# Kernel optimization log

Hardware: AMD Instinct MI355X
Metric: run time of the kernel (lower is better)

Reference implementation:

```python
import jax, jax.numpy as jnp
import numpy as np

EPS = 1e-10
NUM_RELATION = 4
N_NODES = 50000
N_EDGES = 800000
D_IN = 128
D_H = 256


def rgc_layer(x, src, dst, rel, rel_w, rel_b, loop_w, loop_b):
    # torchdrug RelationalGraphConv: scatter-mean per (node, relation), then
    # linear over concatenated per-relation features + self-loop linear + relu.
    N, d = x.shape
    msg = x[src]                                      # [E, d] gather
    idx = dst * NUM_RELATION + rel                    # [E] bucket per (node, relation)
    num_seg = N * NUM_RELATION
    agg = jax.ops.segment_sum(msg, idx, num_segments=num_seg)            # [N*R, d]
    cnt = jax.ops.segment_sum(jnp.ones((msg.shape[0], 1), x.dtype), idx,
                              num_segments=num_seg)                       # [N*R, 1]
    update = (agg / (cnt + EPS)).reshape(N, NUM_RELATION * d)            # [N, R*d]
    out = update @ rel_w + rel_b + x @ loop_w + loop_b                   # [N, d_out]
    return jax.nn.relu(out)


def highway(x, hp_w, hp_b, ht_w, ht_b):
    proj = jax.nn.relu(x @ hp_w + hp_b)
    gate = jax.nn.sigmoid(x @ ht_w + ht_b)
    return gate * proj + (1.0 - gate) * x


def setup_inputs() -> dict:
    key = jax.random.key(0)
    ks = jax.random.split(key, 16)
    s = 0.02
    inp = {
        "x": jax.random.normal(ks[0], (N_NODES, D_IN), dtype=jnp.float32),
        "src": jax.random.randint(ks[1], (N_EDGES,), 0, N_NODES, dtype=jnp.int32),
        "dst": jax.random.randint(ks[2], (N_EDGES,), 0, N_NODES, dtype=jnp.int32),
        "rel": jax.random.randint(ks[3], (N_EDGES,), 0, NUM_RELATION, dtype=jnp.int32),
        # layer 1: RGC(128->256) + Highway(256)
        "rel_w1": jax.random.normal(ks[4], (NUM_RELATION * D_IN, D_H), dtype=jnp.float32) * s,
        "rel_b1": jnp.zeros((D_H,), jnp.float32),
        "loop_w1": jax.random.normal(ks[5], (D_IN, D_H), dtype=jnp.float32) * s,
        "loop_b1": jnp.zeros((D_H,), jnp.float32),
        "hp_w1": jax.random.normal(ks[6], (D_H, D_H), dtype=jnp.float32) * s,
        "hp_b1": jnp.zeros((D_H,), jnp.float32),
        "ht_w1": jax.random.normal(ks[7], (D_H, D_H), dtype=jnp.float32) * s,
        "ht_b1": jnp.full((D_H,), -2.0, jnp.float32),  # transform.bias.data.fill_(-2.0)
        # layer 2: RGC(256->256) + Highway(256)
        "rel_w2": jax.random.normal(ks[8], (NUM_RELATION * D_H, D_H), dtype=jnp.float32) * s,
        "rel_b2": jnp.zeros((D_H,), jnp.float32),
        "loop_w2": jax.random.normal(ks[9], (D_H, D_H), dtype=jnp.float32) * s,
        "loop_b2": jnp.zeros((D_H,), jnp.float32),
        "hp_w2": jax.random.normal(ks[10], (D_H, D_H), dtype=jnp.float32) * s,
        "hp_b2": jnp.zeros((D_H,), jnp.float32),
        "ht_w2": jax.random.normal(ks[11], (D_H, D_H), dtype=jnp.float32) * s,
        "ht_b2": jnp.full((D_H,), -2.0, jnp.float32),
    }
    return inp


def reference(x, src, dst, rel,
              rel_w1, rel_b1, loop_w1, loop_b1, hp_w1, hp_b1, ht_w1, ht_b1,
              rel_w2, rel_b2, loop_w2, loop_b2, hp_w2, hp_b2, ht_w2, ht_b2):
    h = rgc_layer(x, src, dst, rel, rel_w1, rel_b1, loop_w1, loop_b1)
    h = highway(h, hp_w1, hp_b1, ht_w1, ht_b1)
    h = rgc_layer(h, src, dst, rel, rel_w2, rel_b2, loop_w2, loop_b2)
    h = highway(h, hp_w2, hp_b2, ht_w2, ht_b2)
    return h  # node_feature, shape [N, 256]
```

## Files before the change

kernel.cpp:

```cpp
#include <hip/hip_runtime.h>

typedef __bf16 bf16_t;
typedef __bf16 bf16x8 __attribute__((ext_vector_type(8)));
typedef __bf16 bf16x4 __attribute__((ext_vector_type(4)));
typedef float f32x4 __attribute__((ext_vector_type(4)));
typedef int i32x4 __attribute__((ext_vector_type(4)));

#define BM 128
#define BK 64

__device__ __forceinline__ void gload_lds16(const void* g, void* s) {
    __builtin_amdgcn_global_load_lds(
        (const __attribute__((address_space(1))) unsigned int*)g,
        (__attribute__((address_space(3))) unsigned int*)s, 16, 0, 0);
}

__global__ __launch_bounds__(256, 2) void gemm_k(
    const bf16_t* __restrict__ A, int lda, int M,
    const bf16_t* __restrict__ Bt, int K,
    const float* __restrict__ bias, int relu_flag,
    bf16_t* __restrict__ outb, int ldo, int ocol,
    int NTM)
{
    __shared__ __align__(16) bf16_t As[BM * BK];
    __shared__ __align__(16) bf16_t Bs[256 * BK];

    const int L   = blockIdx.x;
    const int xcd = L & 7;
    const int sup = L >> 3;
    const int mt  = sup * 8 + xcd;
    if (mt >= NTM) return;
    const int m0 = mt * BM;

    const int tid  = threadIdx.x;
    const int wave = tid >> 6, lane = tid & 63;
    const int wr   = wave >> 1, wc = wave & 1;
    const int lm   = lane & 15, quad = lane >> 4;

    const bf16_t* ag[4];
    const bf16_t* bg[8];
    #pragma unroll
    for (int j = 0; j < 4; j++) {
        int c   = j * 256 + tid;
        int row = c >> 3;
        int col = ((c & 7) ^ (row & 7)) << 3;
        int gm  = m0 + row; if (gm >= M) gm = M - 1;
        ag[j] = A + (size_t)gm * lda + col;
    }
    #pragma unroll
    for (int j = 0; j < 8; j++) {
        int c   = j * 256 + tid;
        int row = c >> 3;
        int col = ((c & 7) ^ (row & 7)) << 3;
        bg[j] = Bt + (size_t)row * K + col;
    }

    f32x4 acc[4][8] = {};

    for (int k0 = 0; k0 < K; k0 += BK) {
        __syncthreads();
        #pragma unroll
        for (int j = 0; j < 4; j++)
            gload_lds16(ag[j] + k0, As + (size_t)(j * 256 + tid) * 8);
        #pragma unroll
        for (int j = 0; j < 8; j++)
            gload_lds16(bg[j] + k0, Bs + (size_t)(j * 256 + tid) * 8);
        __syncthreads();

        #pragma unroll
        for (int h = 0; h < 2; h++) {
            bf16x8 af[4];
            #pragma unroll
            for (int i = 0; i < 4; i++) {
                int r = wr * 64 + i * 16 + lm;
                af[i] = *(const bf16x8*)&As[(size_t)(r * 8 + ((h * 4 + quad) ^ (r & 7))) * 8];
            }
            #pragma unroll
            for (int ni = 0; ni < 8; ni++) {
                int r = wc * 128 + ni * 16 + lm;
                bf16x8 bfr = *(const bf16x8*)&Bs[(size_t)(r * 8 + ((h * 4 + quad) ^ (r & 7))) * 8];
                #pragma unroll
                for (int mi = 0; mi < 4; mi++)
                    acc[mi][ni] = __builtin_amdgcn_mfma_f32_16x16x32_bf16(
                        af[mi], bfr, acc[mi][ni], 0, 0, 0);
            }
        }
    }

    #pragma unroll
    for (int mi = 0; mi < 4; mi++) {
        #pragma unroll
        for (int ni = 0; ni < 8; ni++) {
            int col = wc * 128 + ni * 16 + lm;
            float b = bias[col];
            #pragma unroll
            for (int r = 0; r < 4; r++) {
                int row = m0 + wr * 64 + mi * 16 + quad * 4 + r;
                if (row < M) {
                    float v = acc[mi][ni][r] + b;
                    if (relu_flag) v = fmaxf(v, 0.f);
                    outb[(size_t)row * ldo + ocol + col] = (bf16_t)v;
                }
            }
        }
    }
}

__global__ __launch_bounds__(256, 2) void gemm_hw2(
    const bf16_t* __restrict__ A, int M,
    const bf16_t* __restrict__ Bt,
    const float* __restrict__ bias,
    bf16_t* __restrict__ outb, int ldo, int ocol,
    float* __restrict__ outf, int NTM)
{
    __shared__ __align__(16) bf16_t As[128 * 64];
    __shared__ __align__(16) bf16_t Bs[256 * 64];

    const int L    = blockIdx.x;
    const int xcd  = L & 7;
    const int rest = L >> 3;
    const int nt   = rest & 1;
    const int sup  = rest >> 1;
    const int mt   = sup * 8 + xcd;
    if (mt >= NTM) return;
    const int m0 = mt * 128;

    const int tid  = threadIdx.x;
    const int wave = tid >> 6, lane = tid & 63;
    const int lm   = lane & 15, quad = lane >> 4;

    const bf16_t* ag[4];
    const bf16_t* bg[8];
    #pragma unroll
    for (int j = 0; j < 4; j++) {
        int c   = j * 256 + tid;
        int row = c >> 3;
        int col = ((c & 7) ^ (row & 7)) << 3;
        int gm  = m0 + row; if (gm >= M) gm = M - 1;
        ag[j] = A + (size_t)gm * 256 + col;
    }
    #pragma unroll
    for (int j = 0; j < 8; j++) {
        int c    = j * 256 + tid;
        int row  = c >> 3;
        int col  = ((c & 7) ^ (row & 7)) << 3;
        int grow = nt * 128 + row + ((row >= 128) ? 128 : 0);
        bg[j] = Bt + (size_t)grow * 256 + col;
    }

    f32x4 acc[2][16] = {};

    for (int k0 = 0; k0 < 256; k0 += 64) {
        __syncthreads();
        #pragma unroll
        for (int j = 0; j < 4; j++)
            gload_lds16(ag[j] + k0, As + (size_t)(j * 256 + tid) * 8);
        #pragma unroll
        for (int j = 0; j < 8; j++)
            gload_lds16(bg[j] + k0, Bs + (size_t)(j * 256 + tid) * 8);
        __syncthreads();

        #pragma unroll
        for (int h = 0; h < 2; h++) {
            bf16x8 af[2];
            #pragma unroll
            for (int i = 0; i < 2; i++) {
                int r = wave * 32 + i * 16 + lm;
                af[i] = *(const bf16x8*)&As[(size_t)(r * 8 + ((h * 4 + quad) ^ (r & 7))) * 8];
            }
            #pragma unroll
            for (int ni = 0; ni < 16; ni++) {
                int r = ni * 16 + lm;
                bf16x8 bfr = *(const bf16x8*)&Bs[(size_t)(r * 8 + ((h * 4 + quad) ^ (r & 7))) * 8];
                #pragma unroll
                for (int mi = 0; mi < 2; mi++)
                    acc[mi][ni] = __builtin_amdgcn_mfma_f32_16x16x32_bf16(
                        af[mi], bfr, acc[mi][ni], 0, 0, 0);
            }
        }
    }

    #pragma unroll
    for (int mi = 0; mi < 2; mi++) {
        #pragma unroll
        for (int ni = 0; ni < 8; ni++) {
            int col = nt * 128 + ni * 16 + lm;
            float bp  = bias[col];
            float bg2 = bias[256 + col];
            #pragma unroll
            for (int r = 0; r < 4; r++) {
                int row = m0 + wave * 32 + mi * 16 + quad * 4 + r;
                if (row < M) {
                    float p = acc[mi][ni][r] + bp;
                    float g = acc[mi][ni + 8][r] + bg2;
                    float s = 1.0f / (1.0f + __expf(-g));
                    float hv = (float)A[(size_t)row * 256 + col];
                    float v = s * fmaxf(p, 0.f) + (1.0f - s) * hv;
                    if (outf) outf[(size_t)row * 256 + col] = v;
                    else      outb[(size_t)row * ldo + ocol + col] = (bf16_t)v;
                }
            }
        }
    }
}

__global__ void prep_all(
    const float* __restrict__ rel_w1, const float* __restrict__ loop_w1,
    const float* __restrict__ rel_w2, const float* __restrict__ loop_w2,
    const float* __restrict__ hp_w1,  const float* __restrict__ ht_w1,
    const float* __restrict__ hp_w2,  const float* __restrict__ ht_w2,
    bf16_t* __restrict__ W1t, bf16_t* __restrict__ W2t,
    bf16_t* __restrict__ Wh1t, bf16_t* __restrict__ Wh2t,
    const float* __restrict__ rb1, const float* __restrict__ lb1,
    const float* __restrict__ rb2, const float* __restrict__ lb2,
    const float* __restrict__ hpb1, const float* __restrict__ htb1,
    const float* __restrict__ hpb2, const float* __restrict__ htb2,
    float* __restrict__ bR1, float* __restrict__ bR2,
    float* __restrict__ bH1, float* __restrict__ bH2,
    const float* __restrict__ x, bf16_t* __restrict__ A1, int N,
    int* __restrict__ cnt, int NSEG, int cvb)
{
    int b = blockIdx.x, tid = threadIdx.x;
    if (b < 2944) {
        const float* W; bf16_t* Wt; int ldk, k0, n0, base;
        if      (b < 512)  { W = rel_w1;  Wt = W1t;  ldk = 640;  k0 = 0;    n0 = 0;   base = 0; }
        else if (b < 640)  { W = loop_w1; Wt = W1t;  ldk = 640;  k0 = 512;  n0 = 0;   base = 512; }
        else if (b < 1664) { W = rel_w2;  Wt = W2t;  ldk = 1280; k0 = 0;    n0 = 0;   base = 640; }
        else if (b < 1920) { W = loop_w2; Wt = W2t;  ldk = 1280; k0 = 1024; n0 = 0;   base = 1664; }
        else if (b < 2176) { W = hp_w1;   Wt = Wh1t; ldk = 256;  k0 = 0;    n0 = 0;   base = 1920; }
        else if (b < 2432) { W = ht_w1;   Wt = Wh1t; ldk = 256;  k0 = 0;    n0 = 256; base = 2176; }
        else if (b < 2688) { W = hp_w2;   Wt = Wh2t; ldk = 256;  k0 = 0;    n0 = 0;   base = 2432; }
        else               { W = ht_w2;   Wt = Wh2t; ldk = 256;  k0 = 0;    n0 = 256; base = 2688; }
        int k = b - base;
        int n = tid;
        Wt[(size_t)(n0 + n) * ldk + k0 + k] = (bf16_t)W[(size_t)k * 256 + n];
    } else if (b == 2944) {
        int t = tid;
        bR1[t] = rb1[t] + lb1[t];
        bR2[t] = rb2[t] + lb2[t];
        bH1[t] = hpb1[t]; bH1[256 + t] = htb1[t];
        bH2[t] = hpb2[t]; bH2[256 + t] = htb2[t];
    } else if (b < 2945 + cvb) {
        int t = (b - 2945) * 256 + tid;
        if (t < N * 32) {
            int row = t >> 5, c = (t & 31) << 2;
            f32x4 v = *(const f32x4*)(x + (size_t)row * 128 + c);
            bf16x4 o;
            o[0] = (bf16_t)v[0]; o[1] = (bf16_t)v[1]; o[2] = (bf16_t)v[2]; o[3] = (bf16_t)v[3];
            *(bf16x4*)(A1 + (size_t)row * 640 + 512 + c) = o;
        }
    } else {
        int t = ((b - 2945 - cvb) * 256 + tid) * 4;
        if (t < NSEG) {
            i32x4 z = {0, 0, 0, 0};
            *(i32x4*)(cnt + t) = z;
        }
    }
}

__global__ void count_k(const int* __restrict__ dst, const int* __restrict__ rel,
                        int* __restrict__ cnt, int E)
{
    int e = blockIdx.x * blockDim.x + threadIdx.x;
    if (e < E) atomicAdd(&cnt[dst[e] * 4 + rel[e]], 1);
}

__global__ void scan_partial(const int* __restrict__ cnt, int* __restrict__ offs,
                             int* __restrict__ chunkSums, int NSEG)
{
    __shared__ int sh[256];
    int t = threadIdx.x;
    int idx = blockIdx.x * 256 + t;
    int v = (idx < NSEG) ? cnt[idx] : 0;
    sh[t] = v;
    __syncthreads();
    for (int d = 1; d < 256; d <<= 1) {
        int add = (t >= d) ? sh[t - d] : 0;
        __syncthreads();
        sh[t] += add;
        __syncthreads();
    }
    if (idx < NSEG) offs[idx] = sh[t] - v;
    if (t == 255) chunkSums[blockIdx.x] = sh[t];
}

__global__ void scan_chunks(int* __restrict__ chunkSums, int NCHUNK)
{
    __shared__ int sh[1024];
    int t = threadIdx.x;
    int v = (t < NCHUNK) ? chunkSums[t] : 0;
    sh[t] = v;
    __syncthreads();
    for (int d = 1; d < 1024; d <<= 1) {
        int add = (t >= d) ? sh[t - d] : 0;
        __syncthreads();
        sh[t] += add;
        __syncthreads();
    }
    if (t < NCHUNK) chunkSums[t] = sh[t] - v;
}

__global__ void scan_add(int* __restrict__ offs, const int* __restrict__ chunkSums,
                         int* __restrict__ cursor, int NSEG)
{
    int idx = blockIdx.x * 256 + threadIdx.x;
    if (idx < NSEG) {
        int o = offs[idx] + chunkSums[blockIdx.x];
        offs[idx] = o;
        cursor[idx] = o;
    }
}

__global__ void fill_k(const int* __restrict__ src, const int* __restrict__ dst,
                       const int* __restrict__ rel,
                       int* __restrict__ cursor, int* __restrict__ eidx, int E)
{
    int e = blockIdx.x * blockDim.x + threadIdx.x;
    if (e < E) {
        int seg = dst[e] * 4 + rel[e];
        int pos = atomicAdd(&cursor[seg], 1);
        eidx[pos] = src[e];
    }
}

__global__ void seg_mean256(const int* __restrict__ offs, const int* __restrict__ cnt,
                            const int* __restrict__ eidx,
                            const bf16_t* __restrict__ xb, int ldx,
                            bf16_t* __restrict__ Aout, int lda, int NSEG)
{
    int wv = (blockIdx.x << 2) + (threadIdx.x >> 6);
    if (wv >= NSEG) return;
    int lane = threadIdx.x & 63;
    int half = lane >> 5;
    int c = (lane & 31) << 3;
    int start = offs[wv];
    int n = cnt[wv];
    float acc[8] = {};
    int i = 0;
    for (; i + 8 <= n; i += 8) {
        int s0 = eidx[start + i + 0 + half];
        int s1 = eidx[start + i + 2 + half];
        int s2 = eidx[start + i + 4 + half];
        int s3 = eidx[start + i + 6 + half];
        bf16x8 v0 = *(const bf16x8*)(xb + (size_t)s0 * ldx + c);
        bf16x8 v1 = *(const bf16x8*)(xb + (size_t)s1 * ldx + c);
        bf16x8 v2 = *(const bf16x8*)(xb + (size_t)s2 * ldx + c);
        bf16x8 v3 = *(const bf16x8*)(xb + (size_t)s3 * ldx + c);
        #pragma unroll
        for (int j = 0; j < 8; j++)
            acc[j] += ((float)v0[j] + (float)v1[j]) + ((float)v2[j] + (float)v3[j]);
    }
    for (; i + 2 <= n; i += 2) {
        int s = eidx[start + i + half];
        bf16x8 v = *(const bf16x8*)(xb + (size_t)s * ldx + c);
        #pragma unroll
        for (int j = 0; j < 8; j++) acc[j] += (float)v[j];
    }
    if (i < n && half == 0) {
        int s = eidx[start + i];
        bf16x8 v = *(const bf16x8*)(xb + (size_t)s * ldx + c);
        #pragma unroll
        for (int j = 0; j < 8; j++) acc[j] += (float)v[j];
    }
    #pragma unroll
    for (int j = 0; j < 8; j++) acc[j] += __shfl_xor(acc[j], 32, 64);
    if (half == 0) {
        float inv = 1.0f / ((float)n + 1e-10f);
        int node = wv >> 2, r = wv & 3;
        bf16x8 o;
        #pragma unroll
        for (int j = 0; j < 8; j++) o[j] = (bf16_t)(acc[j] * inv);
        *(bf16x8*)(Aout + (size_t)node * lda + r * 256 + c) = o;
    }
}

__global__ void seg_mean128(const int* __restrict__ offs, const int* __restrict__ cnt,
                            const int* __restrict__ eidx,
                            const bf16_t* __restrict__ xb, int ldx,
                            bf16_t* __restrict__ Aout, int lda, int NSEG)
{
    int wv = (blockIdx.x << 2) + (threadIdx.x >> 6);
    if (wv >= NSEG) return;
    int lane = threadIdx.x & 63;
    int q = lane >> 4;
    int c = (lane & 15) << 3;
    int start = offs[wv];
    int n = cnt[wv];
    float acc[8] = {};
    int i = 0;
    for (; i + 8 <= n; i += 8) {
        int s0 = eidx[start + i + q];
        int s1 = eidx[start + i + 4 + q];
        bf16x8 v0 = *(const bf16x8*)(xb + (size_t)s0 * ldx + c);
        bf16x8 v1 = *(const bf16x8*)(xb + (size_t)s1 * ldx + c);
        #pragma unroll
        for (int j = 0; j < 8; j++) acc[j] += (float)v0[j] + (float)v1[j];
    }
    for (; i + 4 <= n; i += 4) {
        int s = eidx[start + i + q];
        bf16x8 v = *(const bf16x8*)(xb + (size_t)s * ldx + c);
        #pragma unroll
        for (int j = 0; j < 8; j++) acc[j] += (float)v[j];
    }
    if (q < n - i) {
        int s = eidx[start + i + q];
        bf16x8 v = *(const bf16x8*)(xb + (size_t)s * ldx + c);
        #pragma unroll
        for (int j = 0; j < 8; j++) acc[j] += (float)v[j];
    }
    #pragma unroll
    for (int j = 0; j < 8; j++) {
        acc[j] += __shfl_xor(acc[j], 16, 64);
        acc[j] += __shfl_xor(acc[j], 32, 64);
    }
    if (lane < 16) {
        float inv = 1.0f / ((float)n + 1e-10f);
        int node = wv >> 2, r = wv & 3;
        bf16x8 o;
        #pragma unroll
        for (int j = 0; j < 8; j++) o[j] = (bf16_t)(acc[j] * inv);
        *(bf16x8*)(Aout + (size_t)node * lda + r * 128 + c) = o;
    }
}

extern "C" void kernel_launch(void* const* d_in, const int* in_sizes, int n_in,
                              void* d_out, int out_size, void* d_ws, size_t ws_size,
                              hipStream_t stream)
{
    const float* x       = (const float*)d_in[0];
    const int*   src     = (const int*)d_in[1];
    const int*   dst     = (const int*)d_in[2];
    const int*   rel     = (const int*)d_in[3];
    const float* rel_w1  = (const float*)d_in[4];
    const float* rel_b1  = (const float*)d_in[5];
    const float* loop_w1 = (const float*)d_in[6];
    const float* loop_b1 = (const float*)d_in[7];
    const float* hp_w1   = (const float*)d_in[8];
    const float* hp_b1   = (const float*)d_in[9];
    const float* ht_w1   = (const float*)d_in[10];
    const float* ht_b1   = (const float*)d_in[11];
    const float* rel_w2  = (const float*)d_in[12];
    const float* rel_b2  = (const float*)d_in[13];
    const float* loop_w2 = (const float*)d_in[14];
    const float* loop_b2 = (const float*)d_in[15];
    const float* hp_w2   = (const float*)d_in[16];
    const float* hp_b2   = (const float*)d_in[17];
    const float* ht_w2   = (const float*)d_in[18];
    const float* ht_b2   = (const float*)d_in[19];

    const int N = in_sizes[0] / 128;
    const int E = in_sizes[1];
    const int NSEG = N * 4;
    const int NCHUNK = (NSEG + 255) / 256;
    float* out = (float*)d_out;

    char* ws = (char*)d_ws;
    size_t off = 0;
    auto alloc = [&](size_t bytes) {
        void* p = ws + off;
        off += (bytes + 255) & ~(size_t)255;
        return p;
    };
    int*    cnt    = (int*)alloc((size_t)NSEG * 4);
    int*    offs   = (int*)alloc((size_t)NSEG * 4);
    int*    cursor = (int*)alloc((size_t)NSEG * 4);
    int*    chunkS = (int*)alloc(4096);
    int*    eidx   = (int*)alloc((size_t)E * 4);
    bf16_t* A1     = (bf16_t*)alloc((size_t)N * 640 * 2);
    bf16_t* A2     = (bf16_t*)alloc((size_t)N * 1280 * 2);
    bf16_t* h      = (bf16_t*)alloc((size_t)N * 256 * 2);
    bf16_t* W1t    = (bf16_t*)alloc((size_t)256 * 640 * 2);
    bf16_t* W2t    = (bf16_t*)alloc((size_t)256 * 1280 * 2);
    bf16_t* Wh1t   = (bf16_t*)alloc((size_t)512 * 256 * 2);
    bf16_t* Wh2t   = (bf16_t*)alloc((size_t)512 * 256 * 2);
    float*  bR1    = (float*)alloc(256 * 4);
    float*  bR2    = (float*)alloc(256 * 4);
    float*  bH1    = (float*)alloc(512 * 4);
    float*  bH2    = (float*)alloc(512 * 4);

    dim3 blk(256);
    const int NTM = (N + BM - 1) / BM;
    const int supers = (NTM + 7) / 8;
    const int gridRGC = supers * 8;
    const int gridHW  = supers * 8 * 2;

    const int cvb = (N * 32 + 255) / 256;
    const int zb  = (NSEG / 4 + 255) / 256;
    prep_all<<<dim3(2945 + cvb + zb), blk, 0, stream>>>(
        rel_w1, loop_w1, rel_w2, loop_w2, hp_w1, ht_w1, hp_w2, ht_w2,
        W1t, W2t, Wh1t, Wh2t,
        rel_b1, loop_b1, rel_b2, loop_b2, hp_b1, ht_b1, hp_b2, ht_b2,
        bR1, bR2, bH1, bH2,
        x, A1, N, cnt, NSEG, cvb);

    count_k<<<dim3((E + 255) / 256), blk, 0, stream>>>(dst, rel, cnt, E);
    scan_partial<<<dim3(NCHUNK), blk, 0, stream>>>(cnt, offs, chunkS, NSEG);
    scan_chunks<<<dim3(1), dim3(1024), 0, stream>>>(chunkS, NCHUNK);
    scan_add<<<dim3(NCHUNK), blk, 0, stream>>>(offs, chunkS, cursor, NSEG);
    fill_k<<<dim3((E + 255) / 256), blk, 0, stream>>>(src, dst, rel, cursor, eidx, E);

    seg_mean128<<<dim3((NSEG + 3) / 4), blk, 0, stream>>>(offs, cnt, eidx,
                                                          A1 + 512, 640, A1, 640, NSEG);
    gemm_k<<<dim3(gridRGC), blk, 0, stream>>>(A1, 640, N, W1t, 640,
                                              bR1, 1, h, 256, 0, NTM);
    gemm_hw2<<<dim3(gridHW), blk, 0, stream>>>(h, N, Wh1t, bH1,
                                               A2, 1280, 1024, nullptr, NTM);

    seg_mean256<<<dim3((NSEG + 3) / 4), blk, 0, stream>>>(offs, cnt, eidx,
                                                          A2 + 1024, 1280, A2, 1280, NSEG);
    gemm_k<<<dim3(gridRGC), blk, 0, stream>>>(A2, 1280, N, W2t, 1280,
                                              bR2, 1, h, 256, 0, NTM);
    gemm_hw2<<<dim3(gridHW), blk, 0, stream>>>(h, N, Wh2t, bH2,
                                               nullptr, 0, 0, out, NTM);
}
```

Before: 513.8 us.

## Double-buffer GEMM LDS tiles with BK=32 and batch weight transpose via shared memory

Both GEMM kernels now use two LDS buffers holding K-slices of 32 instead of one 64-wide buffer. The next slice's global loads are issued before computing on the current one, so there is one barrier per iteration instead of two, and a new swizzle maps two rows per 64-element LDS line. Separately, the weight transpose/convert in prep_all now stages 16 K-rows per block in shared memory and writes 16-byte vectors, replacing 2944 scalar-store blocks with 184. The double buffering aims to hide global-to-LDS latency, at the cost of smaller K tiles and more loop iterations.

```diff
diff --git a/kernel.cpp b/kernel.cpp
--- a/kernel.cpp
+++ b/kernel.cpp
@@ -7,12 +7,23 @@
 typedef int i32x4 __attribute__((ext_vector_type(4)));
 
 #define BM 128
-#define BK 64
 
 __device__ __forceinline__ void gload_lds16(const void* g, void* s) {
     __builtin_amdgcn_global_load_lds(
         (const __attribute__((address_space(1))) unsigned int*)g,
         (__attribute__((address_space(3))) unsigned int*)s, 16, 0, 0);
+}
+
+__device__ __forceinline__ void chunk_map(int g, int& row, int& kcol) {
+    int L = g >> 3;
+    int v = (g & 7) ^ (L & 7);
+    row  = 2 * L + (v >> 2);
+    kcol = (v & 3) << 3;
+}
+
+__device__ __forceinline__ int frag_off(int r, int quad) {
+    int L = r >> 1;
+    return L * 64 + (((((r & 1) << 2) | quad) ^ (L & 7)) << 3);
 }
 
 __global__ __launch_bounds__(256, 2) void gemm_k(
@@ -22,8 +33,8 @@
     bf16_t* __restrict__ outb, int ldo, int ocol,
     int NTM)
 {
-    __shared__ __align__(16) bf16_t As[BM * BK];
-    __shared__ __align__(16) bf16_t Bs[256 * BK];
+    __shared__ __align__(16) bf16_t As[2][128 * 32];
+    __shared__ __align__(16) bf16_t Bs[2][256 * 32];
 
     const int L   = blockIdx.x;
     const int xcd = L & 7;
@@ -37,54 +48,56 @@
     const int wr   = wave >> 1, wc = wave & 1;
     const int lm   = lane & 15, quad = lane >> 4;
 
-    const bf16_t* ag[4];
-    const bf16_t* bg[8];
+    const bf16_t* ag[2];
+    const bf16_t* bg[4];
+    #pragma unroll
+    for (int j = 0; j < 2; j++) {
+        int row, kcol; chunk_map(j * 256 + tid, row, kcol);
+        int gm = m0 + row; if (gm >= M) gm = M - 1;
+        ag[j] = A + (size_t)gm * lda + kcol;
+    }
     #pragma unroll
     for (int j = 0; j < 4; j++) {
-        int c   = j * 256 + tid;
-        int row = c >> 3;
-        int col = ((c & 7) ^ (row & 7)) << 3;
-        int gm  = m0 + row; if (gm >= M) gm = M - 1;
-        ag[j] = A + (size_t)gm * lda + col;
-    }
-    #pragma unroll
-    for (int j = 0; j < 8; j++) {
-        int c   = j * 256 + tid;
-        int row = c >> 3;
-        int col = ((c & 7) ^ (row & 7)) << 3;
-        bg[j] = Bt + (size_t)row * K + col;
+        int row, kcol; chunk_map(j * 256 + tid, row, kcol);
+        bg[j] = Bt + (size_t)row * K + kcol;
     }
 
     f32x4 acc[4][8] = {};
-
-    for (int k0 = 0; k0 < K; k0 += BK) {
-        __syncthreads();
-        #pragma unroll
-        for (int j = 0; j < 4; j++)
-            gload_lds16(ag[j] + k0, As + (size_t)(j * 256 + tid) * 8);
-        #pragma unroll
-        for (int j = 0; j < 8; j++)
-            gload_lds16(bg[j] + k0, Bs + (size_t)(j * 256 + tid) * 8);
-        __syncthreads();
-
-        #pragma unroll
-        for (int h = 0; h < 2; h++) {
-            bf16x8 af[4];
-            #pragma unroll
-            for (int i = 0; i < 4; i++) {
-                int r = wr * 64 + i * 16 + lm;
-                af[i] = *(const bf16x8*)&As[(size_t)(r * 8 + ((h * 4 + quad) ^ (r & 7))) * 8];
-            }
-            #pragma unroll
-            for (int ni = 0; ni < 8; ni++) {
-                int r = wc * 128 + ni * 16 + lm;
-                bf16x8 bfr = *(const bf16x8*)&Bs[(size_t)(r * 8 + ((h * 4 + quad) ^ (r & 7))) * 8];
-                #pragma unroll
-                for (int mi = 0; mi < 4; mi++)
-                    acc[mi][ni] = __builtin_amdgcn_mfma_f32_16x16x32_bf16(
-                        af[mi], bfr, acc[mi][ni], 0, 0, 0);
-            }
-        }
+    const int nt = K >> 5;
+
+    #pragma unroll
+    for (int j = 0; j < 2; j++)
+        gload_lds16(ag[j], &As[0][(j * 256 + tid) * 8]);
+    #pragma unroll
+    for (int j = 0; j < 4; j++)
+        gload_lds16(bg[j], &Bs[0][(j * 256 + tid) * 8]);
+    __syncthreads();
+
+    int cur = 0;
+    for (int t = 0; t < nt; ++t) {
+        if (t + 1 < nt) {
+            int k0n = (t + 1) << 5;
+            #pragma unroll
+            for (int j = 0; j < 2; j++)
+                gload_lds16(ag[j] + k0n, &As[cur ^ 1][(j * 256 + tid) * 8]);
+            #pragma unroll
+            for (int j = 0; j < 4; j++)
+                gload_lds16(bg[j] + k0n, &Bs[cur ^ 1][(j * 256 + tid) * 8]);
+        }
+        bf16x8 af[4];
+        #pragma unroll
+        for (int i = 0; i < 4; i++)
+            af[i] = *(const bf16x8*)&As[cur][frag_off(wr * 64 + i * 16 + lm, quad)];
+        #pragma unroll
+        for (int ni = 0; ni < 8; ni++) {
+            bf16x8 bfr = *(const bf16x8*)&Bs[cur][frag_off(wc * 128 + ni * 16 + lm, quad)];
+            #pragma unroll
+            for (int mi = 0; mi < 4; mi++)
+                acc[mi][ni] = __builtin_amdgcn_mfma_f32_16x16x32_bf16(
+                    af[mi], bfr, acc[mi][ni], 0, 0, 0);
+        }
+        __syncthreads();
+        cur ^= 1;
     }
 
     #pragma unroll
@@ -113,13 +126,13 @@
     bf16_t* __restrict__ outb, int ldo, int ocol,
     float* __restrict__ outf, int NTM)
 {
-    __shared__ __align__(16) bf16_t As[128 * 64];
-    __shared__ __align__(16) bf16_t Bs[256 * 64];
+    __shared__ __align__(16) bf16_t As[2][128 * 32];
+    __shared__ __align__(16) bf16_t Bs[2][256 * 32];
 
     const int L    = blockIdx.x;
     const int xcd  = L & 7;
     const int rest = L >> 3;
-    const int nt   = rest & 1;
+    const int nt2  = rest & 1;
     const int sup  = rest >> 1;
     const int mt   = sup * 8 + xcd;
     if (mt >= NTM) return;
@@ -129,62 +142,64 @@
     const int wave = tid >> 6, lane = tid & 63;
     const int lm   = lane & 15, quad = lane >> 4;
 
-    const bf16_t* ag[4];
-    const bf16_t* bg[8];
+    const bf16_t* ag[2];
+    const bf16_t* bg[4];
+    #pragma unroll
+    for (int j = 0; j < 2; j++) {
+        int row, kcol; chunk_map(j * 256 + tid, row, kcol);
+        int gm = m0 + row; if (gm >= M) gm = M - 1;
+        ag[j] = A + (size_t)gm * 256 + kcol;
+    }
     #pragma unroll
     for (int j = 0; j < 4; j++) {
-        int c   = j * 256 + tid;
-        int row = c >> 3;
-        int col = ((c & 7) ^ (row & 7)) << 3;
-        int gm  = m0 + row; if (gm >= M) gm = M - 1;
-        ag[j] = A + (size_t)gm * 256 + col;
-    }
-    #pragma unroll
-    for (int j = 0; j < 8; j++) {
-        int c    = j * 256 + tid;
-        int row  = c >> 3;
-        int col  = ((c & 7) ^ (row & 7)) << 3;
-        int grow = nt * 128 + row + ((row >= 128) ? 128 : 0);
-        bg[j] = Bt + (size_t)grow * 256 + col;
+        int row, kcol; chunk_map(j * 256 + tid, row, kcol);
+        int grow = nt2 * 128 + row + ((row >= 128) ? 128 : 0);
+        bg[j] = Bt + (size_t)grow * 256 + kcol;
     }
 
     f32x4 acc[2][16] = {};
-
-    for (int k0 = 0; k0 < 256; k0 += 64) {
-        __syncthreads();
-        #pragma unroll
-        for (int j = 0; j < 4; j++)
-            gload_lds16(ag[j] + k0, As + (size_t)(j * 256 + tid) * 8);
-        #pragma unroll
-        for (int j = 0; j < 8; j++)
-            gload_lds16(bg[j] + k0, Bs + (size_t)(j * 256 + tid) * 8);
-        __syncthreads();
-
-        #pragma unroll
-        for (int h = 0; h < 2; h++) {
-            bf16x8 af[2];
-            #pragma unroll
-            for (int i = 0; i < 2; i++) {
-                int r = wave * 32 + i * 16 + lm;
-                af[i] = *(const bf16x8*)&As[(size_t)(r * 8 + ((h * 4 + quad) ^ (r & 7))) * 8];
-            }
-            #pragma unroll
-            for (int ni = 0; ni < 16; ni++) {
-                int r = ni * 16 + lm;
-                bf16x8 bfr = *(const bf16x8*)&Bs[(size_t)(r * 8 + ((h * 4 + quad) ^ (r & 7))) * 8];
-                #pragma unroll
-                for (int mi = 0; mi < 2; mi++)
-                    acc[mi][ni] = __builtin_amdgcn_mfma_f32_16x16x32_bf16(
-                        af[mi], bfr, acc[mi][ni], 0, 0, 0);
-            }
-        }
+    const int nt = 8;
+
+    #pragma unroll
+    for (int j = 0; j < 2; j++)
+        gload_lds16(ag[j], &As[0][(j * 256 + tid) * 8]);
+    #pragma unroll
+    for (int j = 0; j < 4; j++)
+        gload_lds16(bg[j], &Bs[0][(j * 256 + tid) * 8]);
+    __syncthreads();
+
+    int cur = 0;
+    for (int t = 0; t < nt; ++t) {
+        if (t + 1 < nt) {
+            int k0n = (t + 1) << 5;
+            #pragma unroll
+            for (int j = 0; j < 2; j++)
+                gload_lds16(ag[j] + k0n, &As[cur ^ 1][(j * 256 + tid) * 8]);
+            #pragma unroll
+            for (int j = 0; j < 4; j++)
+                gload_lds16(bg[j] + k0n, &Bs[cur ^ 1][(j * 256 + tid) * 8]);
+        }
+        bf16x8 af[2];
+        #pragma unroll
+        for (int i = 0; i < 2; i++)
+            af[i] = *(const bf16x8*)&As[cur][frag_off(wave * 32 + i * 16 + lm, quad)];
+        #pragma unroll
+        for (int ni = 0; ni < 16; ni++) {
+            bf16x8 bfr = *(const bf16x8*)&Bs[cur][frag_off(ni * 16 + lm, quad)];
+            #pragma unroll
+            for (int mi = 0; mi < 2; mi++)
+                acc[mi][ni] = __builtin_amdgcn_mfma_f32_16x16x32_bf16(
+                    af[mi], bfr, acc[mi][ni], 0, 0, 0);
+        }
+        __syncthreads();
+        cur ^= 1;
     }
 
     #pragma unroll
     for (int mi = 0; mi < 2; mi++) {
         #pragma unroll
         for (int ni = 0; ni < 8; ni++) {
-            int col = nt * 128 + ni * 16 + lm;
+            int col = nt2 * 128 + ni * 16 + lm;
             float bp  = bias[col];
             float bg2 = bias[256 + col];
             #pragma unroll
@@ -220,28 +235,40 @@
     const float* __restrict__ x, bf16_t* __restrict__ A1, int N,
     int* __restrict__ cnt, int NSEG, int cvb)
 {
+    __shared__ float sh[16][256];
     int b = blockIdx.x, tid = threadIdx.x;
-    if (b < 2944) {
-        const float* W; bf16_t* Wt; int ldk, k0, n0, base;
-        if      (b < 512)  { W = rel_w1;  Wt = W1t;  ldk = 640;  k0 = 0;    n0 = 0;   base = 0; }
-        else if (b < 640)  { W = loop_w1; Wt = W1t;  ldk = 640;  k0 = 512;  n0 = 0;   base = 512; }
-        else if (b < 1664) { W = rel_w2;  Wt = W2t;  ldk = 1280; k0 = 0;    n0 = 0;   base = 640; }
-        else if (b < 1920) { W = loop_w2; Wt = W2t;  ldk = 1280; k0 = 1024; n0 = 0;   base = 1664; }
-        else if (b < 2176) { W = hp_w1;   Wt = Wh1t; ldk = 256;  k0 = 0;    n0 = 0;   base = 1920; }
-        else if (b < 2432) { W = ht_w1;   Wt = Wh1t; ldk = 256;  k0 = 0;    n0 = 256; base = 2176; }
-        else if (b < 2688) { W = hp_w2;   Wt = Wh2t; ldk = 256;  k0 = 0;    n0 = 0;   base = 2432; }
-        else               { W = ht_w2;   Wt = Wh2t; ldk = 256;  k0 = 0;    n0 = 256; base = 2688; }
-        int k = b - base;
-        int n = tid;
-        Wt[(size_t)(n0 + n) * ldk + k0 + k] = (bf16_t)W[(size_t)k * 256 + n];
-    } else if (b == 2944) {
+    if (b < 184) {
+        const float* W; bf16_t* Wt; int ldk, k0, n0, kb;
+        if      (b < 32)  { W = rel_w1;  Wt = W1t;  ldk = 640;  k0 = 0;    n0 = 0;   kb = b; }
+        else if (b < 40)  { W = loop_w1; Wt = W1t;  ldk = 640;  k0 = 512;  n0 = 0;   kb = b - 32; }
+        else if (b < 104) { W = rel_w2;  Wt = W2t;  ldk = 1280; k0 = 0;    n0 = 0;   kb = b - 40; }
+        else if (b < 120) { W = loop_w2; Wt = W2t;  ldk = 1280; k0 = 1024; n0 = 0;   kb = b - 104; }
+        else if (b < 136) { W = hp_w1;   Wt = Wh1t; ldk = 256;  k0 = 0;    n0 = 0;   kb = b - 120; }
+        else if (b < 152) { W = ht_w1;   Wt = Wh1t; ldk = 256;  k0 = 0;    n0 = 256; kb = b - 136; }
+        else if (b < 168) { W = hp_w2;   Wt = Wh2t; ldk = 256;  k0 = 0;    n0 = 0;   kb = b - 152; }
+        else              { W = ht_w2;   Wt = Wh2t; ldk = 256;  k0 = 0;    n0 = 256; kb = b - 168; }
+        int kb16 = kb * 16;
+        #pragma unroll
+        for (int kk = 0; kk < 16; kk++)
+            sh[kk][tid] = W[(size_t)(kb16 + kk) * 256 + tid];
+        __syncthreads();
+        bf16x8 o0, o1;
+        #pragma unroll
+        for (int j = 0; j < 8; j++) {
+            o0[j] = (bf16_t)sh[j][tid];
+            o1[j] = (bf16_t)sh[8 + j][tid];
+        }
+        bf16_t* p = Wt + (size_t)(n0 + tid) * ldk + k0 + kb16;
+        *(bf16x8*)p = o0;
+        *(bf16x8*)(p + 8) = o1;
+    } else if (b == 184) {
         int t = tid;
         bR1[t] = rb1[t] + lb1[t];
         bR2[t] = rb2[t] + lb2[t];
         bH1[t] = hpb1[t]; bH1[256 + t] = htb1[t];
         bH2[t] = hpb2[t]; bH2[256 + t] = htb2[t];
-    } else if (b < 2945 + cvb) {
-        int t = (b - 2945) * 256 + tid;
+    } else if (b < 185 + cvb) {
+        int t = (b - 185) * 256 + tid;
         if (t < N * 32) {
             int row = t >> 5, c = (t & 31) << 2;
             f32x4 v = *(const f32x4*)(x + (size_t)row * 128 + c);
@@ -250,7 +277,7 @@
             *(bf16x4*)(A1 + (size_t)row * 640 + 512 + c) = o;
         }
     } else {
-        int t = ((b - 2945 - cvb) * 256 + tid) * 4;
+        int t = ((b - 185 - cvb) * 256 + tid) * 4;
         if (t < NSEG) {
             i32x4 z = {0, 0, 0, 0};
             *(i32x4*)(cnt + t) = z;
@@ -486,7 +513,7 @@
 
     const int cvb = (N * 32 + 255) / 256;
     const int zb  = (NSEG / 4 + 255) / 256;
-    prep_all<<<dim3(2945 + cvb + zb), blk, 0, stream>>>(
+    prep_all<<<dim3(185 + cvb + zb), blk, 0, stream>>>(
         rel_w1, loop_w1, rel_w2, loop_w2, hp_w1, ht_w1, hp_w2, ht_w2,
         W1t, W2t, Wh1t, Wh2t,
         rel_b1, loop_b1, rel_b2, loop_b2, hp_b1, ht_b1, hp_b2, ht_b2,
```

Result: no change. 515.4 us (+0.3%).
